# Optimization experiments

Hardware: AMD Instinct MI355X
Metric: run time of the kernel (lower is better)

## Reference

```python
import jax, jax.numpy as jnp
import numpy as np

B, N, D_IN, D_EMB = 8, 2048, 768, 768

def setup_inputs() -> dict:
    key = jax.random.key(0)
    k1, k2, k3, k4 = jax.random.split(key, 4)
    x = jax.random.normal(k1, (B, N, D_IN), dtype=jnp.float32)
    # nn.Linear weights stored as [out, in]; applied as x @ W.T
    Wq = jax.random.normal(k2, (D_EMB, D_IN), dtype=jnp.float32) * (D_IN ** -0.5)
    Wk = jax.random.normal(k3, (D_EMB, D_IN), dtype=jnp.float32) * (D_IN ** -0.5)
    Wv = jax.random.normal(k4, (D_EMB, D_IN), dtype=jnp.float32) * (D_IN ** -0.5)
    return {"x": x, "Wq": Wq, "Wk": Wk, "Wv": Wv}

def reference(x, Wq, Wk, Wv):
    dim_sqrt = jnp.asarray(D_EMB ** 0.5, x.dtype)
    q = jnp.einsum('bnd,ed->bne', x, Wq)  # [B,N,E]
    k = jnp.einsum('bnd,ed->bne', x, Wk)
    v = jnp.einsum('bnd,ed->bne', x, Wv)
    scores = jnp.einsum('bne,bme->bnm', q, k)  # [B,N,N]
    # NOTE: module applies softmax FIRST, then divides by sqrt(d) (post-hoc)
    attn = jax.nn.softmax(scores, axis=-1) / dim_sqrt
    out = jnp.einsum('bnm,bme->bne', attn, v)
    return out
```

## Files before the change

### kernel.cpp

```cpp
#include <hip/hip_runtime.h>
#include <stdint.h>
#include <type_traits>

typedef __bf16 bf16;
typedef _Float16 f16;
typedef bf16 bf16x8 __attribute__((ext_vector_type(8)));
typedef f16 f16x8 __attribute__((ext_vector_type(8)));
typedef float f32x4 __attribute__((ext_vector_type(4)));

#define LOG2E 1.4426950408889634f
#define SQRT_E 27.712812921102035f

enum { EPI_F32 = 0, EPI_PAIR = 1, EPI_VT = 2, EPI_F16 = 3 };

__device__ __forceinline__ void async16(const void* g, void* l) {
  __builtin_amdgcn_global_load_lds(
      (__attribute__((address_space(1))) void*)(uintptr_t)g,
      (__attribute__((address_space(3))) void*)l, 16, 0, 0);
}

__device__ __forceinline__ f32x4 mfma8(bf16x8 a, bf16x8 b, f32x4 c) {
  return __builtin_amdgcn_mfma_f32_16x16x32_bf16(a, b, c, 0, 0, 0);
}
__device__ __forceinline__ f32x4 mfma8(f16x8 a, f16x8 b, f32x4 c) {
  return __builtin_amdgcn_mfma_f32_16x16x32_f16(a, b, c, 0, 0, 0);
}

template <int N>
__device__ __forceinline__ void vwait() {
  asm volatile("s_waitcnt vmcnt(%0)" ::"i"(N) : "memory");
}
__device__ __forceinline__ void block_bar() {
  asm volatile("" ::: "memory");
  __builtin_amdgcn_s_barrier();
  asm volatile("" ::: "memory");
}
__device__ __forceinline__ void lgkm0() {
  asm volatile("s_waitcnt lgkmcnt(0)" ::: "memory");
}
__device__ __forceinline__ void spin() { __builtin_amdgcn_sched_barrier(0); }

template <typename T, typename TO, int AT, int EPI>
__global__ __launch_bounds__(512, 2)
void gemm_ring(const T* __restrict__ Ah, const T* __restrict__ Al,
               const T* __restrict__ Bh, void* __restrict__ C0,
               int K, long lda, long ldb, long ldc,
               long stA, long stB, long stC, int gxN, int gyM, int nz) {
  using vec8 = typename std::conditional<std::is_same<T, bf16>::value,
                                         bf16x8, f16x8>::type;
  constexpr int LPT = (AT == 2) ? 6 : 4;
  __shared__ __align__(16) T sA[3][256 * 32];
  __shared__ __align__(16) T sB[3][256 * 32];
  __shared__ __align__(16) T sAl[AT == 2 ? 3 * 256 * 32 : 8];

  const int id = blockIdx.x;
  const int xcd = id & 7;
  const int j0 = id >> 3;
  const int s = j0 / gxN;
  const int bxi = j0 - s * gxN;
  const int g = xcd + 8 * s;
  int byi, z;
  if (nz > 0) { z = g % nz; byi = g / nz; }
  else        { byi = g % gyM; z = g / gyM; }

  const T* pA = Ah + (long)z * stA;
  const T* pB = Bh + (long)z * stB;
  const T* pAl = (AT == 2) ? Al : nullptr;

  const int bm = byi * 256;
  const int bn = bxi * 256;
  const int tid = threadIdx.x;
  const int wave = tid >> 6;
  const int lane = tid & 63;
  const int wm = (wave >> 2) * 128;
  const int wn = (wave & 3) * 64;
  const int quad = lane >> 4;
  const int l16 = lane & 15;

  f32x4 acc[8][4] = {};

  const int srow = tid >> 2;
  const int swc = ((tid & 3) ^ ((tid >> 3) & 3)) * 8;
  const int cread = (quad ^ ((l16 >> 1) & 3)) * 8;

  const int NT = K / 32;

  auto stageA = [&](int buf, int t, int l) {
    const long ka = (long)t * 32 + swc;
    async16(pA + (long)(bm + l * 128 + srow) * lda + ka,
            &sA[buf][(l * 512 + tid) * 8]);
  };
  auto stageB = [&](int buf, int t, int l) {
    const long ka = (long)t * 32 + swc;
    async16(pB + (long)(bn + l * 128 + srow) * ldb + ka,
            &sB[buf][(l * 512 + tid) * 8]);
  };
  auto stageAl = [&](int buf, int t, int l) {
    const long ka = (long)t * 32 + swc;
    async16(pAl + (long)(bm + l * 128 + srow) * lda + ka,
            &sAl[buf * 8192 + (l * 512 + tid) * 8]);
  };

  stageA(0, 0, 0); stageA(0, 0, 1); stageB(0, 0, 0); stageB(0, 0, 1);
  if constexpr (AT == 2) { stageAl(0, 0, 0); stageAl(0, 0, 1); }
  stageA(1, 1, 0); stageA(1, 1, 1); stageB(1, 1, 0); stageB(1, 1, 1);
  if constexpr (AT == 2) { stageAl(1, 1, 0); stageAl(1, 1, 1); }
  vwait<LPT>();
  block_bar();

  int cur = 0, b2 = 2;
  for (int t = 0; t < NT; ++t) {
    const bool st = (t + 2 < NT);
    vec8 bfr[4], af[4], alf[AT == 2 ? 4 : 1];
#pragma unroll
    for (int j = 0; j < 4; ++j)
      bfr[j] = *(const vec8*)&sB[cur][(wn + j * 16 + l16) * 32 + cread];
#pragma unroll
    for (int i = 0; i < 4; ++i) {
      af[i] = *(const vec8*)&sA[cur][(wm + i * 16 + l16) * 32 + cread];
      if constexpr (AT == 2)
        alf[i] = *(const vec8*)&sAl[cur * 8192 + (wm + i * 16 + l16) * 32 + cread];
    }
    if (st) {
      stageA(b2, t + 2, 0); stageA(b2, t + 2, 1);
      if constexpr (AT == 2) stageAl(b2, t + 2, 0);
    }
    block_bar();
    lgkm0();
    spin();
    __builtin_amdgcn_s_setprio(1);
#pragma unroll
    for (int j = 0; j < 4; ++j)
#pragma unroll
      for (int i = 0; i < 4; ++i) {
        acc[i][j] = mfma8(af[i], bfr[j], acc[i][j]);
        if constexpr (AT == 2) acc[i][j] = mfma8(alf[i], bfr[j], acc[i][j]);
      }
    __builtin_amdgcn_s_setprio(0);
    spin();
    block_bar();
    vec8 af2[4], alf2[AT == 2 ? 4 : 1];
#pragma unroll
    for (int i = 0; i < 4; ++i) {
      af2[i] = *(const vec8*)&sA[cur][(wm + 64 + i * 16 + l16) * 32 + cread];
      if constexpr (AT == 2)
        alf2[i] =
            *(const vec8*)&sAl[cur * 8192 + (wm + 64 + i * 16 + l16) * 32 + cread];
    }
    if (st) {
      stageB(b2, t + 2, 0); stageB(b2, t + 2, 1);
      if constexpr (AT == 2) stageAl(b2, t + 2, 1);
    }
    block_bar();
    lgkm0();
    spin();
    __builtin_amdgcn_s_setprio(1);
#pragma unroll
    for (int j = 0; j < 4; ++j)
#pragma unroll
      for (int i = 0; i < 4; ++i) {
        acc[4 + i][j] = mfma8(af2[i], bfr[j], acc[4 + i][j]);
        if constexpr (AT == 2) acc[4 + i][j] = mfma8(alf2[i], bfr[j], acc[4 + i][j]);
      }
    __builtin_amdgcn_s_setprio(0);
    spin();
    if (t + 1 < NT) {
      if (st) vwait<LPT>(); else vwait<0>();
      block_bar();
    }
    cur = (cur == 2) ? 0 : cur + 1;
    b2 = (b2 == 2) ? 0 : b2 + 1;
  }

  if constexpr (EPI == EPI_F32) {
    float* C = (float*)C0 + (long)z * stC;
#pragma unroll
    for (int i = 0; i < 8; ++i) {
      const int mb = bm + wm + i * 16 + quad * 4;
#pragma unroll
      for (int j = 0; j < 4; ++j) {
        const int n = bn + wn + j * 16 + l16;
#pragma unroll
        for (int r = 0; r < 4; ++r)
          C[(long)(mb + r) * ldc + n] = acc[i][j][r];
      }
    }
  } else if constexpr (EPI == EPI_F16) {
    TO* Ch = (TO*)C0;
#pragma unroll
    for (int i = 0; i < 8; ++i) {
      const int mb = bm + wm + i * 16 + quad * 4;
#pragma unroll
      for (int j = 0; j < 4; ++j) {
        const int n = bn + wn + j * 16 + l16;
#pragma unroll
        for (int r = 0; r < 4; ++r)
          Ch[(long)(mb + r) * ldc + n] = (TO)acc[i][j][r];
      }
    }
  } else {
    TO* vT = (TO*)C0;
#pragma unroll
    for (int i = 0; i < 8; ++i) {
      const int mb = bm + wm + i * 16 + quad * 4;
      const long bb = mb >> 11;
      const long ml = mb & 2047;
#pragma unroll
      for (int j = 0; j < 4; ++j) {
        const int e = bn + wn + j * 16 + l16;
        union { TO b[4]; uint2 u; } P;
#pragma unroll
        for (int r = 0; r < 4; ++r) P.b[r] = (TO)acc[i][j][r];
        *(uint2*)&vT[(bb * 768 + e) * 2048 + ml] = P.u;
      }
    }
  }
}

template <typename T, typename TO, int BMt, int BNt, int BKt, int AT, int EPI>
__global__ __launch_bounds__((BMt == 256 ? 512 : 256), 2)
void gemm_pipe(const T* __restrict__ Ah, const T* __restrict__ Al,
               const T* __restrict__ Bh, void* __restrict__ C0,
               int K, long lda, long ldb, long ldc,
               long stA, long stB, long stC, int gxN, int gyM) {
  using vec8 = typename std::conditional<std::is_same<T, bf16>::value,
                                         bf16x8, f16x8>::type;
  static_assert(BMt == BNt, "square tiles only");
  constexpr int THREADS = (BMt == 256) ? 512 : 256;
  constexpr int NWN = (BMt == 256) ? 4 : 2;
  constexpr int WTM = BMt / 2;
  constexpr int WTN = BNt / NWN;
  static_assert(WTN == 64, "wave tile must be 64 wide");
  constexpr int MF = WTM / 16;
  constexpr int KK = BKt / 32;
  constexpr int CPR = BKt / 8;
  constexpr int RPI = THREADS / CPR;
  constexpr int LPP = (BMt * BKt) / (THREADS * 8);
  constexpr int LPT = LPP * (AT == 2 ? 3 : 2);

  __shared__ __align__(16) T sA[2][BMt * BKt];
  __shared__ __align__(16) T sB[2][BNt * BKt];
  __shared__ __align__(16) T sAl[AT == 2 ? 2 * BMt * BKt : 8];

  const int id = blockIdx.x;
  const int xcd = id & 7;
  const int j0 = id >> 3;
  const int s = j0 / gxN;
  const int bxi = j0 - s * gxN;
  const int g = xcd + 8 * s;
  const int byi = g % gyM;
  const int z = g / gyM;

  const T* pA = Ah + (long)z * stA;
  const T* pB = Bh + (long)z * stB;
  const T* pAl = (AT == 2) ? Al : nullptr;

  const int bm = byi * BMt;
  const int bn = bxi * BNt;
  const int tid = threadIdx.x;
  const int wave = tid >> 6;
  const int lane = tid & 63;
  const int wm = (wave / NWN) * WTM;
  const int wn = (wave % NWN) * WTN;
  const int quad = lane >> 4;
  const int l16 = lane & 15;

  f32x4 acc[MF][4] = {};

  const int srow = tid / CPR;
  const int schk = tid % CPR;
  const int swc = ((BKt == 64) ? (schk ^ (srow & 7)) : schk) * 8;
  const int cs0 = (quad * 8) ^ ((BKt == 64) ? ((l16 & 7) << 3) : 0);

  const int NT = K / BKt;

  auto stage = [&](int buf, int t) {
    const long ka = (long)t * BKt + swc;
#pragma unroll
    for (int l = 0; l < LPP; ++l)
      async16(pA + (long)(bm + l * RPI + srow) * lda + ka,
              &sA[buf][(l * THREADS + tid) * 8]);
#pragma unroll
    for (int l = 0; l < LPP; ++l)
      async16(pB + (long)(bn + l * RPI + srow) * ldb + ka,
              &sB[buf][(l * THREADS + tid) * 8]);
    if constexpr (AT == 2) {
#pragma unroll
      for (int l = 0; l < LPP; ++l)
        async16(pAl + (long)(bm + l * RPI + srow) * lda + ka,
                &sAl[buf * BMt * BKt + (l * THREADS + tid) * 8]);
    }
  };

  auto compute = [&](int buf) {
    const T* bA = &sA[buf][0];
    const T* bB = &sB[buf][0];
    const T* bAl = (AT == 2) ? &sAl[buf * BMt * BKt] : nullptr;
    vec8 bf[KK][4];
#pragma unroll
    for (int kk = 0; kk < KK; ++kk)
#pragma unroll
      for (int jj = 0; jj < 4; ++jj)
        bf[kk][jj] =
            *(const vec8*)&bB[(wn + jj * 16 + l16) * BKt + (cs0 ^ (kk * 32))];
#pragma unroll
    for (int mq = 0; mq < MF / 2; ++mq) {
      vec8 af[KK][2];
      vec8 alf[AT == 2 ? KK : 1][2];
#pragma unroll
      for (int kk = 0; kk < KK; ++kk)
#pragma unroll
        for (int ii = 0; ii < 2; ++ii) {
          const int r = wm + mq * 32 + ii * 16 + l16;
          af[kk][ii] = *(const vec8*)&bA[r * BKt + (cs0 ^ (kk * 32))];
          if constexpr (AT == 2)
            alf[kk][ii] = *(const vec8*)&bAl[r * BKt + (cs0 ^ (kk * 32))];
        }
      __builtin_amdgcn_s_setprio(1);
#pragma unroll
      for (int jj = 0; jj < 4; ++jj)
#pragma unroll
        for (int ii = 0; ii < 2; ++ii)
#pragma unroll
          for (int kk = 0; kk < KK; ++kk) {
            acc[mq * 2 + ii][jj] =
                mfma8(af[kk][ii], bf[kk][jj], acc[mq * 2 + ii][jj]);
            if constexpr (AT == 2)
              acc[mq * 2 + ii][jj] =
                  mfma8(alf[kk][ii], bf[kk][jj], acc[mq * 2 + ii][jj]);
          }
      __builtin_amdgcn_s_setprio(0);
    }
  };

  stage(0, 0);
  stage(1, 1);
  vwait<LPT>();
  block_bar();

  for (int t = 0; t < NT; ++t) {
    const int cur = t & 1;
    compute(cur);
    if (t + 1 < NT) {
      block_bar();
      if (t + 2 < NT) {
        stage(cur, t + 2);
        vwait<LPT>();
      } else {
        vwait<0>();
      }
      block_bar();
    }
  }

  if constexpr (EPI == EPI_F16) {
    TO* Ch = (TO*)C0;
#pragma unroll
    for (int i = 0; i < MF; ++i) {
      const int mb = bm + wm + i * 16 + quad * 4;
#pragma unroll
      for (int j = 0; j < 4; ++j) {
        const int n = bn + wn + j * 16 + l16;
#pragma unroll
        for (int r = 0; r < 4; ++r)
          Ch[(long)(mb + r) * ldc + n] = (TO)acc[i][j][r];
      }
    }
  } else if constexpr (EPI == EPI_VT) {
    TO* vT = (TO*)C0;
#pragma unroll
    for (int i = 0; i < MF; ++i) {
      const int mb = bm + wm + i * 16 + quad * 4;
      const long bb = mb >> 11;
      const long ml = mb & 2047;
#pragma unroll
      for (int j = 0; j < 4; ++j) {
        const int e = bn + wn + j * 16 + l16;
        union { TO b[4]; uint2 u; } P;
#pragma unroll
        for (int r = 0; r < 4; ++r) P.b[r] = (TO)acc[i][j][r];
        *(uint2*)&vT[(bb * 768 + e) * 2048 + ml] = P.u;
      }
    }
  } else {
    float* C = (float*)C0 + (long)z * stC;
#pragma unroll
    for (int i = 0; i < MF; ++i) {
      const int mb = bm + wm + i * 16 + quad * 4;
#pragma unroll
      for (int j = 0; j < 4; ++j) {
        const int n = bn + wn + j * 16 + l16;
#pragma unroll
        for (int r = 0; r < 4; ++r)
          C[(long)(mb + r) * ldc + n] = acc[i][j][r];
      }
    }
  }
}

constexpr int BM = 128, BN = 128, BK = 64;

template <typename T, typename TO, int AT, int BT, int EPI, int SWZ>
__global__ __launch_bounds__(256)
void gemm_kernel(const T* __restrict__ Ah, const T* __restrict__ Al,
                 const T* __restrict__ Bh, const T* __restrict__ Bl,
                 void* __restrict__ C0, void* __restrict__ C1,
                 int K, long lda, long ldb, long ldbl, long ldc,
                 long stA, long stB, long stBl, long stC,
                 int gxN, int gyM) {
  using vec8 = typename std::conditional<std::is_same<T, bf16>::value,
                                         bf16x8, f16x8>::type;
  __shared__ __align__(16) T sAh[BM * BK];
  __shared__ __align__(16) T sBh[BN * BK];
  __shared__ __align__(16) T sAl[AT == 2 ? BM * BK : 8];
  __shared__ __align__(16) T sBl[BT == 2 ? BN * BK : 8];

  int bxi, byi, z;
  if constexpr (SWZ) {
    const int id = blockIdx.x;
    const int xcd = id & 7;
    const int j = id >> 3;
    const int s = j / gxN;
    const int n = j - s * gxN;
    const int g = xcd + 8 * s;
    bxi = n;
    byi = g % gyM;
    z = g / gyM;
  } else {
    bxi = blockIdx.x; byi = blockIdx.y; z = blockIdx.z;
  }

  const T* pAh = Ah + (long)z * stA;
  const T* pBh = Bh + (long)z * stB;
  const T* pAl = (AT == 2) ? (Al + (long)z * stA) : nullptr;
  const T* pBl = (BT == 2) ? (Bl + (long)z * stBl) : nullptr;

  const int bm = byi * BM;
  const int bn = bxi * BN;
  const int tid = threadIdx.x;
  const int wave = tid >> 6;
  const int lane = tid & 63;
  const int wm = (wave & 1) * 64;
  const int wn = (wave >> 1) * 64;
  const int quad = lane >> 4;
  const int l16 = lane & 15;

  f32x4 acc[4][4] = {};

  const int sr0 = tid >> 3;
  const int swc = ((tid & 7) ^ (sr0 & 7)) * 8;
  const int cs0 = (quad * 8) ^ ((l16 & 7) << 3);

  for (int kt = 0; kt < K; kt += BK) {
    __syncthreads();
    {
      const long ka = kt + swc;
#pragma unroll
      for (int l = 0; l < 4; ++l) {
        const int row = l * 32 + sr0;
        async16(pAh + (long)(bm + row) * lda + ka, &sAh[(l * 256 + tid) * 8]);
      }
#pragma unroll
      for (int l = 0; l < 4; ++l) {
        const int row = l * 32 + sr0;
        async16(pBh + (long)(bn + row) * ldb + ka, &sBh[(l * 256 + tid) * 8]);
      }
      if constexpr (AT == 2) {
#pragma unroll
        for (int l = 0; l < 4; ++l) {
          const int row = l * 32 + sr0;
          async16(pAl + (long)(bm + row) * lda + ka, &sAl[(l * 256 + tid) * 8]);
        }
      }
      if constexpr (BT == 2) {
#pragma unroll
        for (int l = 0; l < 4; ++l) {
          const int row = l * 32 + sr0;
          async16(pBl + (long)(bn + row) * ldbl + ka, &sBl[(l * 256 + tid) * 8]);
        }
      }
    }
    __syncthreads();

#pragma unroll
    for (int kk = 0; kk < 2; ++kk) {
      const int cs = cs0 ^ (kk * 32);
      vec8 ah[4], al[4];
#pragma unroll
      for (int i = 0; i < 4; ++i) {
        ah[i] = *(const vec8*)&sAh[(wm + i * 16 + l16) * BK + cs];
        if constexpr (AT == 2)
          al[i] = *(const vec8*)&sAl[(wm + i * 16 + l16) * BK + cs];
      }
#pragma unroll
      for (int j = 0; j < 4; ++j) {
        const vec8 bh = *(const vec8*)&sBh[(wn + j * 16 + l16) * BK + cs];
        vec8 bl;
        if constexpr (BT == 2)
          bl = *(const vec8*)&sBl[(wn + j * 16 + l16) * BK + cs];
#pragma unroll
        for (int i = 0; i < 4; ++i) {
          acc[i][j] = mfma8(ah[i], bh, acc[i][j]);
          if constexpr (BT == 2) acc[i][j] = mfma8(ah[i], bl, acc[i][j]);
          if constexpr (AT == 2) acc[i][j] = mfma8(al[i], bh, acc[i][j]);
        }
      }
    }
  }

  if constexpr (EPI == EPI_PAIR) {
    TO* Ch = (TO*)C0;
    TO* Cl = (TO*)C1;
#pragma unroll
    for (int i = 0; i < 4; ++i) {
      const int mb = bm + wm + i * 16 + quad * 4;
#pragma unroll
      for (int j = 0; j < 4; ++j) {
        const int n = bn + wn + j * 16 + l16;
#pragma unroll
        for (int r = 0; r < 4; ++r) {
          const float f = acc[i][j][r];
          const TO h = (TO)f;
          const long idx = (long)(mb + r) * ldc + n;
          Ch[idx] = h;
          Cl[idx] = (TO)(f - (float)h);
        }
      }
    }
  }
}

__global__ __launch_bounds__(256)
void softmax_kernel(float* __restrict__ sc) {
  __shared__ float red[4];
  float* srow = sc + (long)blockIdx.x * 2048;
  const int tid = threadIdx.x;
  const int wave = tid >> 6;
  const int lane = tid & 63;
  const float4 v0 = *(const float4*)(srow + tid * 4);
  const float4 v1 = *(const float4*)(srow + 1024 + tid * 4);
  float mx = fmaxf(fmaxf(fmaxf(v0.x, v0.y), fmaxf(v0.z, v0.w)),
                   fmaxf(fmaxf(v1.x, v1.y), fmaxf(v1.z, v1.w)));
#pragma unroll
  for (int o = 32; o >= 1; o >>= 1) mx = fmaxf(mx, __shfl_xor(mx, o));
  if (lane == 0) red[wave] = mx;
  __syncthreads();
  mx = fmaxf(fmaxf(red[0], red[1]), fmaxf(red[2], red[3]));
  const float e0 = exp2f((v0.x - mx) * LOG2E);
  const float e1 = exp2f((v0.y - mx) * LOG2E);
  const float e2 = exp2f((v0.z - mx) * LOG2E);
  const float e3 = exp2f((v0.w - mx) * LOG2E);
  const float e4 = exp2f((v1.x - mx) * LOG2E);
  const float e5 = exp2f((v1.y - mx) * LOG2E);
  const float e6 = exp2f((v1.z - mx) * LOG2E);
  const float e7 = exp2f((v1.w - mx) * LOG2E);
  float s = ((e0 + e1) + (e2 + e3)) + ((e4 + e5) + (e6 + e7));
#pragma unroll
  for (int o = 32; o >= 1; o >>= 1) s += __shfl_xor(s, o);
  __syncthreads();
  if (lane == 0) red[wave] = s;
  __syncthreads();
  s = red[0] + red[1] + red[2] + red[3];
  const float inv = 1.0f / (s * SQRT_E);
  f16* prow = (f16*)srow;
  union { f16 b[4]; uint2 u; } P;
  P.b[0] = (f16)(e0 * inv); P.b[1] = (f16)(e1 * inv);
  P.b[2] = (f16)(e2 * inv); P.b[3] = (f16)(e3 * inv);
  *(uint2*)(prow + tid * 4) = P.u;
  P.b[0] = (f16)(e4 * inv); P.b[1] = (f16)(e5 * inv);
  P.b[2] = (f16)(e6 * inv); P.b[3] = (f16)(e7 * inv);
  *(uint2*)(prow + 1024 + tid * 4) = P.u;
}

__global__ __launch_bounds__(256)
void split_all(const float4* __restrict__ x, const float4* __restrict__ wv,
               uint2* __restrict__ xh, uint2* __restrict__ xl,
               uint2* __restrict__ wvh) {
  constexpr int NX = 3145728;
  constexpr int NWV = 147456;
  const int i = blockIdx.x * 256 + threadIdx.x;
  float4 v;
  uint2 *dh, *dl;
  if (i < NX) {
    v = x[i]; dh = xh + i; dl = xl + i;
  } else {
    const int m = i - NX;
    if (m >= NWV) return;
    v = wv[m]; dh = wvh + m; dl = nullptr;
  }
  const f16 h0 = (f16)v.x, h1 = (f16)v.y, h2 = (f16)v.z, h3 = (f16)v.w;
  union { f16 b[4]; uint2 u; } P;
  P.b[0] = h0; P.b[1] = h1; P.b[2] = h2; P.b[3] = h3;
  *dh = P.u;
  if (dl != nullptr) {
    P.b[0] = (f16)(v.x - (float)h0);
    P.b[1] = (f16)(v.y - (float)h1);
    P.b[2] = (f16)(v.z - (float)h2);
    P.b[3] = (f16)(v.w - (float)h3);
    *dl = P.u;
  }
}

__global__ __launch_bounds__(256)
void transpose_split(const float* __restrict__ Wq, const float* __restrict__ Wk,
                     f16* __restrict__ qTh, f16* __restrict__ qTl,
                     f16* __restrict__ kTh, f16* __restrict__ kTl) {
  __shared__ float tile[64][65];
  const float* src = blockIdx.z ? Wk : Wq;
  f16* dh = blockIdx.z ? kTh : qTh;
  f16* dl = blockIdx.z ? kTl : qTl;
  const int e0 = blockIdx.y * 64, d0 = blockIdx.x * 64;
  const int t = threadIdx.x;
  const int r = t >> 2;
  const int c4 = (t & 3) * 16;
  const float4* s4 = (const float4*)(src + (long)(e0 + r) * 768 + d0 + c4);
#pragma unroll
  for (int g = 0; g < 4; ++g) {
    const float4 v = s4[g];
    tile[r][c4 + g * 4 + 0] = v.x;
    tile[r][c4 + g * 4 + 1] = v.y;
    tile[r][c4 + g * 4 + 2] = v.z;
    tile[r][c4 + g * 4 + 3] = v.w;
  }
  __syncthreads();
  union { f16 b[8]; uint4 u; } H0, H1, L0, L1;
#pragma unroll
  for (int i = 0; i < 16; ++i) {
    const float v = tile[c4 + i][r];
    const f16 h = (f16)v;
    const f16 l = (f16)(v - (float)h);
    if (i < 8) { H0.b[i] = h; L0.b[i] = l; }
    else       { H1.b[i - 8] = h; L1.b[i - 8] = l; }
  }
  const long o = (long)(d0 + r) * 768 + e0 + c4;
  *(uint4*)(dh + o) = H0.u;  *(uint4*)(dh + o + 8) = H1.u;
  *(uint4*)(dl + o) = L0.u;  *(uint4*)(dl + o + 8) = L1.u;
}

extern "C" void kernel_launch(void* const* d_in, const int* in_sizes, int n_in,
                              void* d_out, int out_size, void* d_ws, size_t ws_size,
                              hipStream_t stream) {
  const float* x  = (const float*)d_in[0];
  const float* Wq = (const float*)d_in[1];
  const float* Wk = (const float*)d_in[2];
  const float* Wv = (const float*)d_in[3];
  float* out = (float*)d_out;
  char* ws = (char*)d_ws;

  const size_t SZ = 25165824;
  f16* yh = (f16*)(ws + 0 * SZ);
  f16* xh = (f16*)(ws + 2 * SZ);
  f16* vT = (f16*)(ws + 3 * SZ);
  const size_t PERS = 4 * SZ;
  const size_t WT = 1179648;
  f16* xl   = (f16*)(ws + PERS);
  f16* wqTh = (f16*)(ws + PERS + SZ);
  f16* wqTl = (f16*)(ws + PERS + SZ + 1 * WT);
  f16* wkTh = (f16*)(ws + PERS + SZ + 2 * WT);
  f16* wkTl = (f16*)(ws + PERS + SZ + 3 * WT);
  f16* mtH  = (f16*)(ws + PERS + SZ + 4 * WT);
  f16* mtL  = (f16*)(ws + PERS + SZ + 5 * WT);
  f16* wvh  = (f16*)(ws + PERS + SZ + 6 * WT);
  float* scores = (float*)(ws + PERS);

  long avail = (long)ws_size - (long)PERS;
  int nb = (int)(avail / 16777216);
  if (nb < 1) nb = 1;
  if (nb > 8) nb = 8;

  split_all<<<12864, 256, 0, stream>>>(
      (const float4*)x, (const float4*)Wv, (uint2*)xh, (uint2*)xl, (uint2*)wvh);
  transpose_split<<<dim3(12, 12, 2), 256, 0, stream>>>(
      Wq, Wk, wqTh, wqTl, wkTh, wkTl);

  gemm_kernel<f16, f16, 2, 2, EPI_PAIR, 0><<<dim3(6, 6, 1), 256, 0, stream>>>(
      wkTh, wkTl, wqTh, wqTl, (void*)mtH, (void*)mtL,
      768, 768, 768, 768, 768, 0, 0, 0, 0, 0, 0);

  gemm_pipe<f16, f16, 128, 128, 32, 2, EPI_F16><<<768, 256, 0, stream>>>(
      xh, xl, mtH, (void*)yh, 768, 768, 768, 768, 0, 0, 0, 6, 128);

  gemm_pipe<f16, f16, 128, 128, 64, 1, EPI_VT><<<768, 256, 0, stream>>>(
      xh, nullptr, wvh, (void*)vT, 768, 768, 768, 0, 0, 0, 0, 6, 128);

  const long RS = 1572864;
  const long VTS = 1572864;
  for (int b0 = 0; b0 < 8; b0 += nb) {
    const int nbg = (8 - b0 < nb) ? (8 - b0) : nb;
    gemm_ring<f16, float, 1, EPI_F32><<<64 * nbg, 512, 0, stream>>>(
        yh + (long)b0 * RS, nullptr, xh + (long)b0 * RS, (void*)scores,
        768, 768, 768, 2048, RS, RS, 4194304L, 8, 8, nbg);
    softmax_kernel<<<nbg * 2048, 256, 0, stream>>>(scores);
    gemm_ring<f16, float, 1, EPI_F32><<<24 * nbg, 512, 0, stream>>>(
        (const f16*)scores, nullptr, vT + (long)b0 * VTS,
        (void*)(out + (long)b0 * 1572864),
        2048, 4096, 2048, 768, 8388608L, VTS, 1572864L, 3, 8, nbg);
  }
}
```

Baseline: 366.1 us.

## Fuse softmax into score GEMM epilogue with split-max rescaling in PV GEMM

The separate fp32 score write and softmax pass are replaced. The QK GEMM epilogue now computes per-tile row max and sum, writes unnormalised exp values as f16, and stores the partial statistics. A small combine kernel turns these into per-tile scale factors, and a new pv_pipe GEMM applies them per 256-column K chunk while accumulating. It also drops the batch-chunk loop so all batches launch at once. The aim is to remove the fp32 score round trip and the standalone softmax kernel, at the cost of an extra rescale step in the PV loop and separate accumulators.

```diff
diff --git a/kernel.cpp b/kernel.cpp
--- a/kernel.cpp
+++ b/kernel.cpp
@@ -40,12 +40,13 @@
 }
 __device__ __forceinline__ void spin() { __builtin_amdgcn_sched_barrier(0); }
 
-template <typename T, typename TO, int AT, int EPI>
+template <typename T, int AT>
 __global__ __launch_bounds__(512, 2)
 void gemm_ring(const T* __restrict__ Ah, const T* __restrict__ Al,
                const T* __restrict__ Bh, void* __restrict__ C0,
                int K, long lda, long ldb, long ldc,
-               long stA, long stB, long stC, int gxN, int gyM, int nz) {
+               long stA, long stB, long stC, int gxN, int gyM, int nz,
+               float* __restrict__ mxg, float* __restrict__ smg) {
   using vec8 = typename std::conditional<std::is_same<T, bf16>::value,
                                          bf16x8, f16x8>::type;
   constexpr int LPT = (AT == 2) ? 6 : 4;
@@ -172,47 +173,238 @@
     b2 = (b2 == 2) ? 0 : b2 + 1;
   }
 
-  if constexpr (EPI == EPI_F32) {
-    float* C = (float*)C0 + (long)z * stC;
-#pragma unroll
-    for (int i = 0; i < 8; ++i) {
-      const int mb = bm + wm + i * 16 + quad * 4;
-#pragma unroll
-      for (int j = 0; j < 4; ++j) {
-        const int n = bn + wn + j * 16 + l16;
+  block_bar();
+  float* red = (float*)(&sA[0][0]);
+  const int wnid = wave & 3;
+  float m_[8][4];
+  {
+    float mx_[8][4];
+#pragma unroll
+    for (int i = 0; i < 8; ++i)
+#pragma unroll
+      for (int r = 0; r < 4; ++r) {
+        float v = fmaxf(fmaxf(acc[i][0][r], acc[i][1][r]),
+                        fmaxf(acc[i][2][r], acc[i][3][r]));
+#pragma unroll
+        for (int o = 8; o >= 1; o >>= 1) v = fmaxf(v, __shfl_xor(v, o));
+        mx_[i][r] = v;
+      }
+    if (l16 == 0) {
+#pragma unroll
+      for (int i = 0; i < 8; ++i)
 #pragma unroll
         for (int r = 0; r < 4; ++r)
-          C[(long)(mb + r) * ldc + n] = acc[i][j][r];
-      }
-    }
-  } else if constexpr (EPI == EPI_F16) {
-    TO* Ch = (TO*)C0;
-#pragma unroll
-    for (int i = 0; i < 8; ++i) {
-      const int mb = bm + wm + i * 16 + quad * 4;
-#pragma unroll
-      for (int j = 0; j < 4; ++j) {
-        const int n = bn + wn + j * 16 + l16;
+          red[(wm + i * 16 + quad * 4 + r) * 4 + wnid] = mx_[i][r];
+    }
+  }
+  block_bar();
+#pragma unroll
+  for (int i = 0; i < 8; ++i)
+#pragma unroll
+    for (int r = 0; r < 4; ++r) {
+      const f32x4 v = *(const f32x4*)&red[(wm + i * 16 + quad * 4 + r) * 4];
+      m_[i][r] = fmaxf(fmaxf(v[0], v[1]), fmaxf(v[2], v[3]));
+    }
+  {
+    float sm_[8][4];
+#pragma unroll
+    for (int i = 0; i < 8; ++i)
+#pragma unroll
+      for (int r = 0; r < 4; ++r) {
+        float ssum = 0.f;
+#pragma unroll
+        for (int j = 0; j < 4; ++j) {
+          const float e = exp2f((acc[i][j][r] - m_[i][r]) * LOG2E);
+          acc[i][j][r] = e;
+          ssum += e;
+        }
+#pragma unroll
+        for (int o = 8; o >= 1; o >>= 1) ssum += __shfl_xor(ssum, o);
+        sm_[i][r] = ssum;
+      }
+    if (l16 == 0) {
+#pragma unroll
+      for (int i = 0; i < 8; ++i)
 #pragma unroll
         for (int r = 0; r < 4; ++r)
-          Ch[(long)(mb + r) * ldc + n] = (TO)acc[i][j][r];
-      }
-    }
-  } else {
-    TO* vT = (TO*)C0;
-#pragma unroll
-    for (int i = 0; i < 8; ++i) {
-      const int mb = bm + wm + i * 16 + quad * 4;
-      const long bb = mb >> 11;
-      const long ml = mb & 2047;
-#pragma unroll
-      for (int j = 0; j < 4; ++j) {
-        const int e = bn + wn + j * 16 + l16;
-        union { TO b[4]; uint2 u; } P;
-#pragma unroll
-        for (int r = 0; r < 4; ++r) P.b[r] = (TO)acc[i][j][r];
-        *(uint2*)&vT[(bb * 768 + e) * 2048 + ml] = P.u;
-      }
+          red[1024 + (wm + i * 16 + quad * 4 + r) * 4 + wnid] = sm_[i][r];
+    }
+  }
+  block_bar();
+  if (wnid == 0 && l16 == 0) {
+    float* mxo = mxg + ((long)z * 8 + bxi) * 2048 + bm;
+    float* smo = smg + ((long)z * 8 + bxi) * 2048 + bm;
+#pragma unroll
+    for (int i = 0; i < 8; ++i)
+#pragma unroll
+      for (int r = 0; r < 4; ++r) {
+        const int row = wm + i * 16 + quad * 4 + r;
+        const f32x4 v = *(const f32x4*)&red[1024 + row * 4];
+        mxo[row] = m_[i][r];
+        smo[row] = (v[0] + v[1]) + (v[2] + v[3]);
+      }
+  }
+  f16* P = (f16*)C0 + (long)z * stC;
+#pragma unroll
+  for (int i = 0; i < 8; ++i) {
+#pragma unroll
+    for (int r = 0; r < 4; ++r) {
+      const long grow = bm + wm + i * 16 + quad * 4 + r;
+#pragma unroll
+      for (int j = 0; j < 4; ++j)
+        P[grow * 2048 + bn + wn + j * 16 + l16] = (f16)acc[i][j][r];
+    }
+  }
+}
+
+__global__ __launch_bounds__(256)
+void combine(const float* __restrict__ mxg, const float* __restrict__ smg,
+             float* __restrict__ gam) {
+  const int R = blockIdx.x * 256 + threadIdx.x;
+  const int z = R >> 11, m = R & 2047;
+  float mx[8], sm[8];
+#pragma unroll
+  for (int t = 0; t < 8; ++t) {
+    mx[t] = mxg[((long)z * 8 + t) * 2048 + m];
+    sm[t] = smg[((long)z * 8 + t) * 2048 + m];
+  }
+  float M = mx[0];
+#pragma unroll
+  for (int t = 1; t < 8; ++t) M = fmaxf(M, mx[t]);
+  float S = 0.f;
+#pragma unroll
+  for (int t = 0; t < 8; ++t) S += sm[t] * exp2f((mx[t] - M) * LOG2E);
+  const float inv = 1.0f / (S * SQRT_E);
+#pragma unroll
+  for (int t = 0; t < 8; ++t)
+    gam[(long)t * 16384 + R] = exp2f((mx[t] - M) * LOG2E) * inv;
+}
+
+__global__ __launch_bounds__(256, 2)
+void pv_pipe(const f16* __restrict__ Pt, const f16* __restrict__ Vt,
+             const float* __restrict__ gam, float* __restrict__ out) {
+  constexpr int LPT = 8;
+  __shared__ __align__(16) f16 sA[2][128 * 64];
+  __shared__ __align__(16) f16 sB[2][128 * 64];
+
+  const int id = blockIdx.x;
+  const int xcd = id & 7;
+  const int j0 = id >> 3;
+  const int s = j0 / 6;
+  const int bxi = j0 - s * 6;
+  const int g = xcd + 8 * s;
+  const int byi = g & 15;
+  const int z = g >> 4;
+
+  const f16* pA = Pt + (long)z * 4194304;
+  const f16* pB = Vt + (long)z * 1572864;
+
+  const int bm = byi * 128;
+  const int bn = bxi * 128;
+  const int tid = threadIdx.x;
+  const int wave = tid >> 6;
+  const int lane = tid & 63;
+  const int wm = (wave >> 1) * 64;
+  const int wn = (wave & 1) * 64;
+  const int quad = lane >> 4;
+  const int l16 = lane & 15;
+
+  f32x4 accM[4][4] = {};
+  f32x4 accT[4][4] = {};
+
+  const int srow = tid >> 3;
+  const int schk = tid & 7;
+  const int swc = (schk ^ (srow & 7)) * 8;
+  const int cs0 = (quad * 8) ^ ((l16 & 7) << 3);
+
+  auto stage = [&](int buf, int t) {
+    const long ka = (long)t * 64 + swc;
+#pragma unroll
+    for (int l = 0; l < 4; ++l)
+      async16(pA + (long)(bm + l * 32 + srow) * 2048 + ka,
+              &sA[buf][(l * 256 + tid) * 8]);
+#pragma unroll
+    for (int l = 0; l < 4; ++l)
+      async16(pB + (long)(bn + l * 32 + srow) * 2048 + ka,
+              &sB[buf][(l * 256 + tid) * 8]);
+  };
+
+  auto compute = [&](int buf) {
+    f16x8 bf[2][4];
+#pragma unroll
+    for (int kk = 0; kk < 2; ++kk)
+#pragma unroll
+      for (int jj = 0; jj < 4; ++jj)
+        bf[kk][jj] = *(const f16x8*)&sB[buf][(wn + jj * 16 + l16) * 64 +
+                                            (cs0 ^ (kk * 32))];
+#pragma unroll
+    for (int mq = 0; mq < 2; ++mq) {
+      f16x8 af[2][2];
+#pragma unroll
+      for (int kk = 0; kk < 2; ++kk)
+#pragma unroll
+        for (int ii = 0; ii < 2; ++ii)
+          af[kk][ii] =
+              *(const f16x8*)&sA[buf][(wm + mq * 32 + ii * 16 + l16) * 64 +
+                                      (cs0 ^ (kk * 32))];
+      __builtin_amdgcn_s_setprio(1);
+#pragma unroll
+      for (int jj = 0; jj < 4; ++jj)
+#pragma unroll
+        for (int ii = 0; ii < 2; ++ii)
+#pragma unroll
+          for (int kk = 0; kk < 2; ++kk)
+            accT[mq * 2 + ii][jj] =
+                mfma8(af[kk][ii], bf[kk][jj], accT[mq * 2 + ii][jj]);
+      __builtin_amdgcn_s_setprio(0);
+    }
+  };
+
+  stage(0, 0);
+  stage(1, 1);
+  vwait<LPT>();
+  block_bar();
+
+  f32x4 gv[4];
+  constexpr int NT = 32;
+  for (int t = 0; t < NT; ++t) {
+    const int cur = t & 1;
+    if ((t & 3) == 0) {
+      const float* gp = gam + ((long)(t >> 2) * 16384 + z * 2048 + bm + wm);
+#pragma unroll
+      for (int i = 0; i < 4; ++i)
+        gv[i] = *(const f32x4*)&gp[i * 16 + quad * 4];
+    }
+    compute(cur);
+    if ((t & 3) == 3) {
+#pragma unroll
+      for (int i = 0; i < 4; ++i)
+#pragma unroll
+        for (int j = 0; j < 4; ++j)
+#pragma unroll
+          for (int r = 0; r < 4; ++r) {
+            accM[i][j][r] += gv[i][r] * accT[i][j][r];
+            accT[i][j][r] = 0.f;
+          }
+    }
+    if (t + 1 < NT) {
+      block_bar();
+      if (t + 2 < NT) { stage(cur, t + 2); vwait<LPT>(); }
+      else vwait<0>();
+      block_bar();
+    }
+  }
+
+  float* C = out + (long)z * 1572864;
+#pragma unroll
+  for (int i = 0; i < 4; ++i) {
+    const int mb = bm + wm + i * 16 + quad * 4;
+#pragma unroll
+    for (int j = 0; j < 4; ++j) {
+      const int n = bn + wn + j * 16 + l16;
+#pragma unroll
+      for (int r = 0; r < 4; ++r)
+        C[(long)(mb + r) * 768 + n] = accM[i][j][r];
     }
   }
 }
@@ -531,48 +723,6 @@
 }
 
 __global__ __launch_bounds__(256)
-void softmax_kernel(float* __restrict__ sc) {
-  __shared__ float red[4];
-  float* srow = sc + (long)blockIdx.x * 2048;
-  const int tid = threadIdx.x;
-  const int wave = tid >> 6;
-  const int lane = tid & 63;
-  const float4 v0 = *(const float4*)(srow + tid * 4);
-  const float4 v1 = *(const float4*)(srow + 1024 + tid * 4);
-  float mx = fmaxf(fmaxf(fmaxf(v0.x, v0.y), fmaxf(v0.z, v0.w)),
-                   fmaxf(fmaxf(v1.x, v1.y), fmaxf(v1.z, v1.w)));
-#pragma unroll
-  for (int o = 32; o >= 1; o >>= 1) mx = fmaxf(mx, __shfl_xor(mx, o));
-  if (lane == 0) red[wave] = mx;
-  __syncthreads();
-  mx = fmaxf(fmaxf(red[0], red[1]), fmaxf(red[2], red[3]));
-  const float e0 = exp2f((v0.x - mx) * LOG2E);
-  const float e1 = exp2f((v0.y - mx) * LOG2E);
-  const float e2 = exp2f((v0.z - mx) * LOG2E);
-  const float e3 = exp2f((v0.w - mx) * LOG2E);
-  const float e4 = exp2f((v1.x - mx) * LOG2E);
-  const float e5 = exp2f((v1.y - mx) * LOG2E);
-  const float e6 = exp2f((v1.z - mx) * LOG2E);
-  const float e7 = exp2f((v1.w - mx) * LOG2E);
-  float s = ((e0 + e1) + (e2 + e3)) + ((e4 + e5) + (e6 + e7));
-#pragma unroll
-  for (int o = 32; o >= 1; o >>= 1) s += __shfl_xor(s, o);
-  __syncthreads();
-  if (lane == 0) red[wave] = s;
-  __syncthreads();
-  s = red[0] + red[1] + red[2] + red[3];
-  const float inv = 1.0f / (s * SQRT_E);
-  f16* prow = (f16*)srow;
-  union { f16 b[4]; uint2 u; } P;
-  P.b[0] = (f16)(e0 * inv); P.b[1] = (f16)(e1 * inv);
-  P.b[2] = (f16)(e2 * inv); P.b[3] = (f16)(e3 * inv);
-  *(uint2*)(prow + tid * 4) = P.u;
-  P.b[0] = (f16)(e4 * inv); P.b[1] = (f16)(e5 * inv);
-  P.b[2] = (f16)(e6 * inv); P.b[3] = (f16)(e7 * inv);
-  *(uint2*)(prow + 1024 + tid * 4) = P.u;
-}
-
-__global__ __launch_bounds__(256)
 void split_all(const float4* __restrict__ x, const float4* __restrict__ wv,
                uint2* __restrict__ xh, uint2* __restrict__ xl,
                uint2* __restrict__ wvh) {
@@ -661,12 +811,10 @@
   f16* mtH  = (f16*)(ws + PERS + SZ + 4 * WT);
   f16* mtL  = (f16*)(ws + PERS + SZ + 5 * WT);
   f16* wvh  = (f16*)(ws + PERS + SZ + 6 * WT);
-  float* scores = (float*)(ws + PERS);
-
-  long avail = (long)ws_size - (long)PERS;
-  int nb = (int)(avail / 16777216);
-  if (nb < 1) nb = 1;
-  if (nb > 8) nb = 8;
+  f16* Pt = (f16*)(ws + PERS);
+  float* mxg = (float*)(ws + PERS + 67108864);
+  float* smg = mxg + 131072;
+  float* gam = smg + 131072;
 
   split_all<<<12864, 256, 0, stream>>>(
       (const float4*)x, (const float4*)Wv, (uint2*)xh, (uint2*)xl, (uint2*)wvh);
@@ -684,16 +832,9 @@
       xh, nullptr, wvh, (void*)vT, 768, 768, 768, 0, 0, 0, 0, 6, 128);
 
   const long RS = 1572864;
-  const long VTS = 1572864;
-  for (int b0 = 0; b0 < 8; b0 += nb) {
-    const int nbg = (8 - b0 < nb) ? (8 - b0) : nb;
-    gemm_ring<f16, float, 1, EPI_F32><<<64 * nbg, 512, 0, stream>>>(
-        yh + (long)b0 * RS, nullptr, xh + (long)b0 * RS, (void*)scores,
-        768, 768, 768, 2048, RS, RS, 4194304L, 8, 8, nbg);
-    softmax_kernel<<<nbg * 2048, 256, 0, stream>>>(scores);
-    gemm_ring<f16, float, 1, EPI_F32><<<24 * nbg, 512, 0, stream>>>(
-        (const f16*)scores, nullptr, vT + (long)b0 * VTS,
-        (void*)(out + (long)b0 * 1572864),
-        2048, 4096, 2048, 768, 8388608L, VTS, 1572864L, 3, 8, nbg);
-  }
-}
+  gemm_ring<f16, 1><<<512, 512, 0, stream>>>(
+      yh, nullptr, xh, (void*)Pt, 768, 768, 768, 2048,
+      RS, RS, 4194304L, 8, 8, 8, mxg, smg);
+  combine<<<64, 256, 0, stream>>>(mxg, smg, gam);
+  pv_pipe<<<768, 256, 0, stream>>>(Pt, vT, gam, out);
+}
```

Measured after the change: 399.8 us. 9.2% more time.
